# Optimization experiments

Hardware: AMD Instinct MI355X
Metric: run time of the kernel (lower is better)

## Reference

```python
import jax, jax.numpy as jnp
import numpy as np

B, T, D_IN = 512, 128, 256
H1, H2 = 1024, 1024
LABEL_DIM = 3


def _lstm_layer(x, W, U, b):
    """Run one keras-LSTMCell layer over x: [T, B, D_in] -> [T, B, H].

    Keras gate order is (i, f, g, o); c' = f*c + i*tanh(g); h = o*tanh(c').
    """
    H = U.shape[0]
    batch = x.shape[1]

    def step(carry, xt):
        h, c = carry
        z = xt @ W + h @ U + b  # [B, 4H]
        i, f, g, o = jnp.split(z, 4, axis=-1)
        i = jax.nn.sigmoid(i)
        f = jax.nn.sigmoid(f)
        g = jnp.tanh(g)
        o = jax.nn.sigmoid(o)
        c_new = f * c + i * g
        h_new = o * jnp.tanh(c_new)
        return (h_new, c_new), h_new

    init = (jnp.zeros((batch, H), x.dtype), jnp.zeros((batch, H), x.dtype))
    _, hs = jax.lax.scan(step, init, x)
    return hs  # [T, B, H]


def setup_inputs() -> dict:
    key = jax.random.key(0)
    ks = jax.random.split(key, 10)
    chars = jax.random.normal(ks[0], (B, T, D_IN), dtype=jnp.float32)
    # sequence lengths in [1, T] so sequence_length - 1 is a valid index
    sequence_length = jax.random.randint(ks[1], (B,), 1, T + 1)
    s = 0.05
    W1 = jax.random.normal(ks[2], (D_IN, 4 * H1), dtype=jnp.float32) * s
    U1 = jax.random.normal(ks[3], (H1, 4 * H1), dtype=jnp.float32) * s
    b1 = jnp.zeros((4 * H1,), dtype=jnp.float32)
    W2 = jax.random.normal(ks[4], (H1, 4 * H2), dtype=jnp.float32) * s
    U2 = jax.random.normal(ks[5], (H2, 4 * H2), dtype=jnp.float32) * s
    b2 = jnp.zeros((4 * H2,), dtype=jnp.float32)
    Wd = jax.random.normal(ks[6], (H2, LABEL_DIM), dtype=jnp.float32) * s
    bd = jnp.zeros((LABEL_DIM,), dtype=jnp.float32)
    return {"chars": chars, "sequence_length": sequence_length,
            "W1": W1, "U1": U1, "b1": b1,
            "W2": W2, "U2": U2, "b2": b2,
            "Wd": Wd, "bd": bd}


def reference(chars, sequence_length, W1, U1, b1, W2, U2, b2, Wd, bd):
    # chars: [B, T, 256] -> time-major [T, B, 256]
    x = jnp.transpose(chars, (1, 0, 2))
    x = _lstm_layer(x, W1, U1, b1)          # [T, B, H1]
    x = _lstm_layer(x, W2, U2, b2)          # [T, B, H2]
    # gather the hidden state at the last valid timestep of each sequence
    batch = chars.shape[0]
    hidden = x[sequence_length - 1, jnp.arange(batch)]  # [B, H2]
    return jax.nn.relu(hidden @ Wd + bd)    # [B, label_dim]
```

## Files before the change

### kernel.cpp

```cpp
#include <hip/hip_runtime.h>
#include <hip/hip_bf16.h>


typedef __hip_bfloat16 bf16;
typedef __attribute__((ext_vector_type(8))) short bfrag8;
typedef __attribute__((ext_vector_type(4))) float accf4;

#define BATCH 512
#define TSTEPS 128
#define DIN 256
#define H 1024
#define NG 4096

__device__ __forceinline__ float sigm(float x) { return 1.0f / (1.0f + __expf(-x)); }
__device__ __forceinline__ float tanh_f(float x) {
    float a = fabsf(x);
    float e = __expf(-2.0f * a);
    float t = (1.0f - e) / (1.0f + e);
    return x < 0.0f ? -t : t;
}
__device__ __forceinline__ unsigned short bfr16(float x) {
    bf16 h = __float2bfloat16(x);
    return *(unsigned short*)&h;
}
__device__ __forceinline__ void gll16(const void* g, void* l) {
    __builtin_amdgcn_global_load_lds(
        (const __attribute__((address_space(1))) unsigned int*)g,
        (__attribute__((address_space(3))) unsigned int*)l, 16, 0, 0);
}

__global__ void k_repack(const float* __restrict__ W, const float* __restrict__ U,
                         bf16* __restrict__ Bp, int KIN)
{
    __shared__ float tile[64][65];
    int kt = blockIdx.x, nt = blockIdx.y;
    int lane = threadIdx.x;
    int n = nt * 64 + lane;
    int orig = ((n >> 5) & 3) * 1024 + (n >> 7) * 32 + (n & 31);
    for (int j = 0; j < 64; ++j) {
        int k = kt * 64 + j;
        tile[j][lane] = (k < KIN) ? W[(size_t)k * NG + orig]
                                  : U[(size_t)(k - KIN) * NG + orig];
    }
    __syncthreads();
    for (int p = 0; p < 8; ++p) {
        int nloc = p * 8 + (lane >> 3);
        int nn = nt * 64 + nloc;
        int kc = lane & 7;
        alignas(16) unsigned short pk[8];
        #pragma unroll
        for (int jj = 0; jj < 8; ++jj) pk[jj] = bfr16(tile[kc * 8 + jj][nloc]);
        *(int4*)(Bp + ((size_t)kt * NG + nn) * 64 + ((kc ^ (nn & 7)) << 3)) = *(int4*)pk;
    }
}

struct StepJob {
    const float* Xf;
    const bf16* A0;
    const bf16* A1;
    const bf16* Bp;
    const float* bias;
    float* C;
    bf16* Hout;
    float* hidden;
    const int* seqlen;
    int xstride;
    int ksplit;
    int KT;
    int t;
};

__global__ __launch_bounds__(256, 2) void k_step(StepJob j0, StepJob j1)
{
    __shared__ __align__(16) bf16 Alds[64 * 64];
    __shared__ __align__(16) bf16 Blds[128 * 64];
    __shared__ float zlds[64][129];

    const StepJob jb = (blockIdx.x >> 8) ? j1 : j0;
    int bi = blockIdx.x & 255;
    int tid = threadIdx.x;
    int wv = tid >> 6, lane = tid & 63;
    int ntile = bi & 31;
    int b0 = (bi >> 5) * 64;
    int n0 = ntile * 128;
    int mw = (wv & 1) * 32;
    int nw = (wv >> 1) * 64;

    const accf4 zero4 = {0.f, 0.f, 0.f, 0.f};
    accf4 acc[2][4];
    #pragma unroll
    for (int i = 0; i < 2; ++i)
        #pragma unroll
        for (int j = 0; j < 4; ++j) acc[i][j] = zero4;

    for (int kt = 0; kt < jb.KT; ++kt) {
        int k0 = kt << 6;
        if (jb.Xf && k0 < jb.ksplit) {
            #pragma unroll
            for (int uu = 0; uu < 2; ++uu) {
                int u = uu * 256 + tid;
                int r = u >> 3;
                int pos = u & 7;
                int kc = pos ^ (r & 7);
                const float* src = jb.Xf + (size_t)(b0 + r) * jb.xstride + k0 + kc * 8;
                float4 va = *(const float4*)src;
                float4 vb = *(const float4*)(src + 4);
                alignas(16) unsigned short pk[8];
                pk[0] = bfr16(va.x); pk[1] = bfr16(va.y);
                pk[2] = bfr16(va.z); pk[3] = bfr16(va.w);
                pk[4] = bfr16(vb.x); pk[5] = bfr16(vb.y);
                pk[6] = bfr16(vb.z); pk[7] = bfr16(vb.w);
                *(int4*)((char*)Alds + u * 16) = *(int4*)pk;
            }
        } else {
            const bf16* Asrc; int kk0;
            if (k0 < jb.ksplit) { Asrc = jb.A0; kk0 = k0; }
            else                { Asrc = jb.A1; kk0 = k0 - jb.ksplit; }
            #pragma unroll
            for (int cc = 0; cc < 2; ++cc) {
                int ob = wv * 2048 + cc * 1024;
                int o = ob + lane * 16;
                int r = o >> 7;
                const char* g = (const char*)(Asrc + (size_t)(b0 + r) * H + kk0) + (o & 127);
                gll16(g, (char*)Alds + ob);
            }
        }
        const char* Bg = (const char*)(jb.Bp + ((size_t)kt * NG + n0) * 64);
        #pragma unroll
        for (int cc = 0; cc < 4; ++cc) {
            int ob = wv * 4096 + cc * 1024;
            gll16(Bg + ob + lane * 16, (char*)Blds + ob);
        }
        __syncthreads();
        #pragma unroll
        for (int kk = 0; kk < 64; kk += 32) {
            int lc = (kk >> 3) + (lane >> 4);
            int ra = mw + (lane & 15);
            int pa = (lc ^ (ra & 7)) << 3;
            bfrag8 af0 = *(const bfrag8*)(Alds + ra * 64 + pa);
            bfrag8 af1 = *(const bfrag8*)(Alds + (ra + 16) * 64 + pa);
            #pragma unroll
            for (int nt = 0; nt < 4; ++nt) {
                int nn = nw + nt * 16 + (lane & 15);
                bfrag8 bfv = *(const bfrag8*)(Blds + nn * 64 + ((lc ^ (nn & 7)) << 3));
                acc[0][nt] = __builtin_amdgcn_mfma_f32_16x16x32_bf16(af0, bfv, acc[0][nt], 0, 0, 0);
                acc[1][nt] = __builtin_amdgcn_mfma_f32_16x16x32_bf16(af1, bfv, acc[1][nt], 0, 0, 0);
            }
        }
        __syncthreads();
    }

    #pragma unroll
    for (int mt = 0; mt < 2; ++mt) {
        int rb = mw + mt * 16 + (lane >> 4) * 4;
        #pragma unroll
        for (int nt = 0; nt < 4; ++nt) {
            int col = nw + nt * 16 + (lane & 15);
            #pragma unroll
            for (int r = 0; r < 4; ++r) zlds[rb + r][col] = acc[mt][nt][r];
        }
    }
    __syncthreads();

    int j = tid & 31;
    int jg = ntile * 32 + j;
    float bi_ = jb.bias[jg], bf_ = jb.bias[H + jg];
    float bg_ = jb.bias[2 * H + jg], bo_ = jb.bias[3 * H + jg];
    int seg = jg & ~63;
    int kc = (jg >> 3) & 7;
    int jl = jg & 7;
    int r0 = (tid >> 5) * 8;
    #pragma unroll
    for (int rr = 0; rr < 8; ++rr) {
        int r = r0 + rr;
        int b = b0 + r;
        float zi = zlds[r][j]      + bi_;
        float zf = zlds[r][32 + j] + bf_;
        float zg = zlds[r][64 + j] + bg_;
        float zo = zlds[r][96 + j] + bo_;
        float ig = sigm(zi), fg = sigm(zf), gv = tanh_f(zg), og = sigm(zo);
        size_t ci = (size_t)b * H + jg;
        float c = fg * jb.C[ci] + ig * gv;
        jb.C[ci] = c;
        float h = og * tanh_f(c);
        int off = seg + ((kc ^ (b & 7)) << 3) + jl;
        jb.Hout[(size_t)b * H + off] = __float2bfloat16(h);
        if (jb.hidden) {
            if (jb.seqlen[b] - 1 == jb.t) jb.hidden[ci] = h;
        }
    }
}

__global__ void k_final(const float* __restrict__ hidden, const float* __restrict__ Wd,
                        const float* __restrict__ bd, float* __restrict__ out)
{
    int b = blockIdx.x;
    int l = threadIdx.x;
    float p0 = 0.f, p1 = 0.f, p2 = 0.f;
    for (int jj = l; jj < H; jj += 64) {
        float hv = hidden[(size_t)b * H + jj];
        p0 += hv * Wd[jj * 3 + 0];
        p1 += hv * Wd[jj * 3 + 1];
        p2 += hv * Wd[jj * 3 + 2];
    }
    #pragma unroll
    for (int off = 32; off > 0; off >>= 1) {
        p0 += __shfl_down(p0, off);
        p1 += __shfl_down(p1, off);
        p2 += __shfl_down(p2, off);
    }
    if (l == 0) {
        out[b * 3 + 0] = fmaxf(p0 + bd[0], 0.f);
        out[b * 3 + 1] = fmaxf(p1 + bd[1], 0.f);
        out[b * 3 + 2] = fmaxf(p2 + bd[2], 0.f);
    }
}

extern "C" void kernel_launch(void* const* d_in, const int* in_sizes, int n_in,
                              void* d_out, int out_size, void* d_ws, size_t ws_size,
                              hipStream_t stream)
{
    const float* chars = (const float*)d_in[0];
    const int* seqlen  = (const int*)d_in[1];
    const float* W1 = (const float*)d_in[2];
    const float* U1 = (const float*)d_in[3];
    const float* b1 = (const float*)d_in[4];
    const float* W2 = (const float*)d_in[5];
    const float* U2 = (const float*)d_in[6];
    const float* b2 = (const float*)d_in[7];
    const float* Wd = (const float*)d_in[8];
    const float* bd = (const float*)d_in[9];
    float* out = (float*)d_out;

    char* ws = (char*)d_ws;
    size_t off = 0;
    bf16* Bp1 = (bf16*)(ws + off); off += (size_t)20 * NG * 64 * 2;
    bf16* Bp2 = (bf16*)(ws + off); off += (size_t)32 * NG * 64 * 2;
    bf16* h1  = (bf16*)(ws + off); off += (size_t)2 * BATCH * H * 2;
    bf16* h2  = (bf16*)(ws + off); off += (size_t)2 * BATCH * H * 2;
    float* c1 = (float*)(ws + off); off += (size_t)BATCH * H * 4;
    float* c2 = (float*)(ws + off); off += (size_t)BATCH * H * 4;
    float* hidden = (float*)(ws + off); off += (size_t)BATCH * H * 4;
    if (ws_size < off) return;

    hipMemsetAsync(h1, 0, (size_t)2 * BATCH * H * 2, stream);
    hipMemsetAsync(h2, 0, (size_t)2 * BATCH * H * 2, stream);
    hipMemsetAsync(c1, 0, (size_t)BATCH * H * 4, stream);
    hipMemsetAsync(c2, 0, (size_t)BATCH * H * 4, stream);

    k_repack<<<dim3(20, 64), 64, 0, stream>>>(W1, U1, Bp1, 256);
    k_repack<<<dim3(32, 64), 64, 0, stream>>>(W2, U2, Bp2, 1024);

    const size_t HS = (size_t)BATCH * H;

    auto mkL1 = [&](int s) {
        StepJob J;
        J.Xf = chars + (size_t)s * DIN;  J.xstride = TSTEPS * DIN;
        J.A0 = nullptr;
        J.A1 = h1 + (size_t)((s + 1) & 1) * HS;
        J.Bp = Bp1; J.bias = b1; J.C = c1;
        J.Hout = h1 + (size_t)(s & 1) * HS;
        J.hidden = nullptr; J.seqlen = nullptr;
        J.ksplit = 256; J.KT = 20; J.t = s;
        return J;
    };
    auto mkL2 = [&](int s) {
        StepJob J;
        J.Xf = nullptr; J.xstride = 0;
        J.A0 = h1 + (size_t)(s & 1) * HS;
        J.A1 = h2 + (size_t)((s + 1) & 1) * HS;
        J.Bp = Bp2; J.bias = b2; J.C = c2;
        J.Hout = h2 + (size_t)(s & 1) * HS;
        J.hidden = hidden; J.seqlen = seqlen;
        J.ksplit = 1024; J.KT = 32; J.t = s;
        return J;
    };

    StepJob first = mkL1(0);
    k_step<<<256, 256, 0, stream>>>(first, first);
    for (int t = 0; t < TSTEPS - 1; ++t) {
        k_step<<<512, 256, 0, stream>>>(mkL2(t), mkL1(t + 1));
    }
    StepJob last = mkL2(TSTEPS - 1);
    k_step<<<256, 256, 0, stream>>>(last, last);
    k_final<<<512, 64, 0, stream>>>(hidden, Wd, bd, out);
}
```

Baseline: 4.181 ms.

## Double K-tile to 128 and fuse gate epilogue directly from MFMA registers

Doubles the K tile from 64 to 128, halving the number of K iterations and barrier pairs per step, and changes the weight repack layout to match. The repack also permutes gate columns so each wave's four N-subtiles hold the i/f/g/o gates for the same hidden units. The LSTM cell epilogue can then run directly from accumulator registers, dropping the zlds shared-memory staging and its barrier. The cost is about 48KB of LDS per block, which may limit occupancy, and the epilogue store pattern for C/H changes.

```diff
diff --git a/kernel.cpp b/kernel.cpp
--- a/kernel.cpp
+++ b/kernel.cpp
@@ -32,25 +32,27 @@
 __global__ void k_repack(const float* __restrict__ W, const float* __restrict__ U,
                          bf16* __restrict__ Bp, int KIN)
 {
-    __shared__ float tile[64][65];
+    __shared__ float tile[128][65];
     int kt = blockIdx.x, nt = blockIdx.y;
     int lane = threadIdx.x;
     int n = nt * 64 + lane;
-    int orig = ((n >> 5) & 3) * 1024 + (n >> 7) * 32 + (n & 31);
-    for (int j = 0; j < 64; ++j) {
-        int k = kt * 64 + j;
+    int orig = ((n >> 4) & 3) * 1024 + (n >> 7) * 32 + ((n >> 6) & 1) * 16 + (n & 15);
+    for (int j = 0; j < 128; ++j) {
+        int k = kt * 128 + j;
         tile[j][lane] = (k < KIN) ? W[(size_t)k * NG + orig]
                                   : U[(size_t)(k - KIN) * NG + orig];
     }
     __syncthreads();
-    for (int p = 0; p < 8; ++p) {
-        int nloc = p * 8 + (lane >> 3);
+    for (int u = 0; u < 16; ++u) {
+        int cid = u * 64 + lane;
+        int nloc = cid >> 4;
+        int pos = cid & 15;
         int nn = nt * 64 + nloc;
-        int kc = lane & 7;
+        int kc = pos ^ (nn & 7);
         alignas(16) unsigned short pk[8];
         #pragma unroll
         for (int jj = 0; jj < 8; ++jj) pk[jj] = bfr16(tile[kc * 8 + jj][nloc]);
-        *(int4*)(Bp + ((size_t)kt * NG + nn) * 64 + ((kc ^ (nn & 7)) << 3)) = *(int4*)pk;
+        *(int4*)(Bp + ((size_t)kt * NG + nn) * 128 + pos * 8) = *(int4*)pk;
     }
 }
 
@@ -72,9 +74,8 @@
 
 __global__ __launch_bounds__(256, 2) void k_step(StepJob j0, StepJob j1)
 {
-    __shared__ __align__(16) bf16 Alds[64 * 64];
-    __shared__ __align__(16) bf16 Blds[128 * 64];
-    __shared__ float zlds[64][129];
+    __shared__ __align__(16) bf16 Alds[64 * 128];
+    __shared__ __align__(16) bf16 Blds[128 * 128];
 
     const StepJob jb = (blockIdx.x >> 8) ? j1 : j0;
     int bi = blockIdx.x & 255;
@@ -85,6 +86,7 @@
     int n0 = ntile * 128;
     int mw = (wv & 1) * 32;
     int nw = (wv >> 1) * 64;
+    int c = lane & 15, q = lane >> 4;
 
     const accf4 zero4 = {0.f, 0.f, 0.f, 0.f};
     accf4 acc[2][4];
@@ -94,13 +96,13 @@
         for (int j = 0; j < 4; ++j) acc[i][j] = zero4;
 
     for (int kt = 0; kt < jb.KT; ++kt) {
-        int k0 = kt << 6;
+        int k0 = kt << 7;
         if (jb.Xf && k0 < jb.ksplit) {
             #pragma unroll
-            for (int uu = 0; uu < 2; ++uu) {
+            for (int uu = 0; uu < 4; ++uu) {
                 int u = uu * 256 + tid;
-                int r = u >> 3;
-                int pos = u & 7;
+                int r = u >> 4;
+                int pos = u & 15;
                 int kc = pos ^ (r & 7);
                 const float* src = jb.Xf + (size_t)(b0 + r) * jb.xstride + k0 + kc * 8;
                 float4 va = *(const float4*)src;
@@ -117,32 +119,32 @@
             if (k0 < jb.ksplit) { Asrc = jb.A0; kk0 = k0; }
             else                { Asrc = jb.A1; kk0 = k0 - jb.ksplit; }
             #pragma unroll
-            for (int cc = 0; cc < 2; ++cc) {
-                int ob = wv * 2048 + cc * 1024;
+            for (int cc = 0; cc < 4; ++cc) {
+                int ob = wv * 4096 + cc * 1024;
                 int o = ob + lane * 16;
-                int r = o >> 7;
-                const char* g = (const char*)(Asrc + (size_t)(b0 + r) * H + kk0) + (o & 127);
+                int r = o >> 8;
+                const char* g = (const char*)Asrc + (size_t)(b0 + r) * (H * 2) + kk0 * 2 + (o & 255);
                 gll16(g, (char*)Alds + ob);
             }
         }
-        const char* Bg = (const char*)(jb.Bp + ((size_t)kt * NG + n0) * 64);
-        #pragma unroll
-        for (int cc = 0; cc < 4; ++cc) {
-            int ob = wv * 4096 + cc * 1024;
+        const char* Bg = (const char*)jb.Bp + ((size_t)kt * NG + n0) * 256;
+        #pragma unroll
+        for (int cc = 0; cc < 8; ++cc) {
+            int ob = wv * 8192 + cc * 1024;
             gll16(Bg + ob + lane * 16, (char*)Blds + ob);
         }
         __syncthreads();
         #pragma unroll
-        for (int kk = 0; kk < 64; kk += 32) {
-            int lc = (kk >> 3) + (lane >> 4);
-            int ra = mw + (lane & 15);
-            int pa = (lc ^ (ra & 7)) << 3;
-            bfrag8 af0 = *(const bfrag8*)(Alds + ra * 64 + pa);
-            bfrag8 af1 = *(const bfrag8*)(Alds + (ra + 16) * 64 + pa);
+        for (int kk = 0; kk < 128; kk += 32) {
+            int kc = (kk >> 3) + q;
+            int ra = mw + c;
+            int pa = (kc ^ (ra & 7)) << 3;
+            bfrag8 af0 = *(const bfrag8*)(Alds + ra * 128 + pa);
+            bfrag8 af1 = *(const bfrag8*)(Alds + (ra + 16) * 128 + pa);
             #pragma unroll
             for (int nt = 0; nt < 4; ++nt) {
-                int nn = nw + nt * 16 + (lane & 15);
-                bfrag8 bfv = *(const bfrag8*)(Blds + nn * 64 + ((lc ^ (nn & 7)) << 3));
+                int nn = nw + nt * 16 + c;
+                bfrag8 bfv = *(const bfrag8*)(Blds + nn * 128 + ((kc ^ (nn & 7)) << 3));
                 acc[0][nt] = __builtin_amdgcn_mfma_f32_16x16x32_bf16(af0, bfv, acc[0][nt], 0, 0, 0);
                 acc[1][nt] = __builtin_amdgcn_mfma_f32_16x16x32_bf16(af1, bfv, acc[1][nt], 0, 0, 0);
             }
@@ -150,43 +152,29 @@
         __syncthreads();
     }
 
+    int hcol = ntile * 32 + (wv >> 1) * 16 + c;
+    float bi_ = jb.bias[hcol],         bf_ = jb.bias[H + hcol];
+    float bg_ = jb.bias[2 * H + hcol], bo_ = jb.bias[3 * H + hcol];
+    int seg = hcol & ~127;
+    int kc_ = (hcol & 127) >> 3;
+    int jl = hcol & 7;
     #pragma unroll
     for (int mt = 0; mt < 2; ++mt) {
-        int rb = mw + mt * 16 + (lane >> 4) * 4;
-        #pragma unroll
-        for (int nt = 0; nt < 4; ++nt) {
-            int col = nw + nt * 16 + (lane & 15);
-            #pragma unroll
-            for (int r = 0; r < 4; ++r) zlds[rb + r][col] = acc[mt][nt][r];
-        }
-    }
-    __syncthreads();
-
-    int j = tid & 31;
-    int jg = ntile * 32 + j;
-    float bi_ = jb.bias[jg], bf_ = jb.bias[H + jg];
-    float bg_ = jb.bias[2 * H + jg], bo_ = jb.bias[3 * H + jg];
-    int seg = jg & ~63;
-    int kc = (jg >> 3) & 7;
-    int jl = jg & 7;
-    int r0 = (tid >> 5) * 8;
-    #pragma unroll
-    for (int rr = 0; rr < 8; ++rr) {
-        int r = r0 + rr;
-        int b = b0 + r;
-        float zi = zlds[r][j]      + bi_;
-        float zf = zlds[r][32 + j] + bf_;
-        float zg = zlds[r][64 + j] + bg_;
-        float zo = zlds[r][96 + j] + bo_;
-        float ig = sigm(zi), fg = sigm(zf), gv = tanh_f(zg), og = sigm(zo);
-        size_t ci = (size_t)b * H + jg;
-        float c = fg * jb.C[ci] + ig * gv;
-        jb.C[ci] = c;
-        float h = og * tanh_f(c);
-        int off = seg + ((kc ^ (b & 7)) << 3) + jl;
-        jb.Hout[(size_t)b * H + off] = __float2bfloat16(h);
-        if (jb.hidden) {
-            if (jb.seqlen[b] - 1 == jb.t) jb.hidden[ci] = h;
+        #pragma unroll
+        for (int reg = 0; reg < 4; ++reg) {
+            int b = b0 + mw + mt * 16 + q * 4 + reg;
+            float ig = sigm(acc[mt][0][reg] + bi_);
+            float fg = sigm(acc[mt][1][reg] + bf_);
+            float gv = tanh_f(acc[mt][2][reg] + bg_);
+            float og = sigm(acc[mt][3][reg] + bo_);
+            size_t ci = (size_t)b * H + hcol;
+            float cv = fg * jb.C[ci] + ig * gv;
+            jb.C[ci] = cv;
+            float h = og * tanh_f(cv);
+            jb.Hout[(size_t)b * H + seg + ((kc_ ^ (b & 7)) << 3) + jl] = __float2bfloat16(h);
+            if (jb.hidden) {
+                if (jb.seqlen[b] - 1 == jb.t) jb.hidden[ci] = h;
+            }
         }
     }
 }
@@ -234,8 +222,8 @@
 
     char* ws = (char*)d_ws;
     size_t off = 0;
-    bf16* Bp1 = (bf16*)(ws + off); off += (size_t)20 * NG * 64 * 2;
-    bf16* Bp2 = (bf16*)(ws + off); off += (size_t)32 * NG * 64 * 2;
+    bf16* Bp1 = (bf16*)(ws + off); off += (size_t)10 * NG * 128 * 2;
+    bf16* Bp2 = (bf16*)(ws + off); off += (size_t)16 * NG * 128 * 2;
     bf16* h1  = (bf16*)(ws + off); off += (size_t)2 * BATCH * H * 2;
     bf16* h2  = (bf16*)(ws + off); off += (size_t)2 * BATCH * H * 2;
     float* c1 = (float*)(ws + off); off += (size_t)BATCH * H * 4;
@@ -248,8 +236,8 @@
     hipMemsetAsync(c1, 0, (size_t)BATCH * H * 4, stream);
     hipMemsetAsync(c2, 0, (size_t)BATCH * H * 4, stream);
 
-    k_repack<<<dim3(20, 64), 64, 0, stream>>>(W1, U1, Bp1, 256);
-    k_repack<<<dim3(32, 64), 64, 0, stream>>>(W2, U2, Bp2, 1024);
+    k_repack<<<dim3(10, 64), 64, 0, stream>>>(W1, U1, Bp1, 256);
+    k_repack<<<dim3(16, 64), 64, 0, stream>>>(W2, U2, Bp2, 1024);
 
     const size_t HS = (size_t)BATCH * H;
 
@@ -261,7 +249,7 @@
         J.Bp = Bp1; J.bias = b1; J.C = c1;
         J.Hout = h1 + (size_t)(s & 1) * HS;
         J.hidden = nullptr; J.seqlen = nullptr;
-        J.ksplit = 256; J.KT = 20; J.t = s;
+        J.ksplit = 256; J.KT = 10; J.t = s;
         return J;
     };
     auto mkL2 = [&](int s) {
@@ -272,7 +260,7 @@
         J.Bp = Bp2; J.bias = b2; J.C = c2;
         J.Hout = h2 + (size_t)(s & 1) * HS;
         J.hidden = hidden; J.seqlen = seqlen;
-        J.ksplit = 1024; J.KT = 32; J.t = s;
+        J.ksplit = 1024; J.KT = 16; J.t = s;
         return J;
     };
 
```

Result: faster. 3.660 ms (-12.5%).
